# Performance work log

Hardware: AMD Instinct MI355X
Metric: run time of the kernel (lower is better)

The kernel has to match this reference:

```python
import jax, jax.numpy as jnp
import numpy as np
from jax import lax

# sign binarization to {-1,+1} with straight-through estimator (standard BNN binarizePM1)
@jax.custom_vjp
def binarize(x):
    return jnp.where(x >= 0, 1.0, -1.0).astype(x.dtype)

def _bin_fwd(x):
    return binarize(x), None

def _bin_bwd(_, g):
    return (g,)  # straight-through

binarize.defvjp(_bin_fwd, _bin_bwd)

def conv2d(x, w, b):
    # NCHW, OIHW, 3x3, stride 1, pad 1
    y = lax.conv_general_dilated(x, w, window_strides=(1, 1), padding=((1, 1), (1, 1)),
                                 dimension_numbers=('NCHW', 'OIHW', 'NCHW'))
    return y + b[None, :, None, None]

def maxpool2(x):
    return lax.reduce_window(x, -jnp.inf, lax.max, (1, 1, 2, 2), (1, 1, 2, 2), 'VALID')

def bn(x, gamma, beta, mean, var, eps=1e-5):
    # inference-mode batchnorm; broadcasts over channel axis 1 (4D) or feature axis 1 (2D)
    if x.ndim == 4:
        shp = (1, -1, 1, 1)
    else:
        shp = (1, -1)
    inv = gamma * lax.rsqrt(var + eps)
    return x * inv.reshape(shp) + (beta - mean * inv).reshape(shp)

def setup_inputs() -> dict:
    key = jax.random.key(0)
    ks = jax.random.split(key, 16)
    B = 4096
    d = {}
    d['x'] = jax.random.normal(ks[0], (B, 1, 28, 28), jnp.float32)
    d['conv1_w'] = jax.random.normal(ks[1], (64, 1, 3, 3), jnp.float32) * 0.1
    d['conv1_b'] = jax.random.normal(ks[2], (64,), jnp.float32) * 0.01
    d['conv2_w'] = jax.random.normal(ks[3], (64, 64, 3, 3), jnp.float32) * 0.05
    d['conv2_b'] = jax.random.normal(ks[4], (64,), jnp.float32) * 0.01
    d['fc1_w'] = jax.random.normal(ks[5], (2048, 7 * 7 * 64), jnp.float32) * 0.02
    d['fc1_b'] = jax.random.normal(ks[6], (2048,), jnp.float32) * 0.01
    d['fc2_w'] = jax.random.normal(ks[7], (10, 2048), jnp.float32) * 0.02
    d['fc2_b'] = jax.random.normal(ks[8], (10,), jnp.float32) * 0.01
    for i, (name, c) in enumerate([('bn1', 64), ('bn2', 64), ('bn3', 2048)]):
        d[name + '_gamma'] = jnp.ones((c,), jnp.float32)
        d[name + '_beta'] = jnp.zeros((c,), jnp.float32)
        d[name + '_mean'] = jax.random.normal(ks[9 + i], (c,), jnp.float32) * 0.1
        d[name + '_var'] = jax.random.uniform(ks[12 + i], (c,), jnp.float32, 0.5, 1.5)
    d['scale'] = jnp.array([1e-5], jnp.float32)
    return d

def reference(x, conv1_w, conv1_b, conv2_w, conv2_b, fc1_w, fc1_b, fc2_w, fc2_b,
              bn1_gamma, bn1_beta, bn1_mean, bn1_var,
              bn2_gamma, bn2_beta, bn2_mean, bn2_var,
              bn3_gamma, bn3_beta, bn3_mean, bn3_var, scale):
    h = conv2d(x, binarize(conv1_w), conv1_b)          # [B,64,28,28]
    h = maxpool2(h)                                    # [B,64,14,14]
    h = bn(h, bn1_gamma, bn1_beta, bn1_mean, bn1_var)
    h = jnp.clip(h, -1.0, 1.0)                         # hardtanh
    h = binarize(h)                                    # qact1
    h = conv2d(h, binarize(conv2_w), conv2_b)          # [B,64,14,14]
    h = maxpool2(h)                                    # [B,64,7,7]
    h = bn(h, bn2_gamma, bn2_beta, bn2_mean, bn2_var)
    h = jnp.clip(h, -1.0, 1.0)
    h = binarize(h)
    h = h.reshape(h.shape[0], -1)                      # [B,3136]
    h = h @ binarize(fc1_w).T + fc1_b                  # [B,2048]
    h = bn(h, bn3_gamma, bn3_beta, bn3_mean, bn3_var)
    h = jnp.clip(h, -1.0, 1.0)
    h = binarize(h)
    h = h @ binarize(fc2_w).T + fc2_b                  # [B,10]
    return h * scale
```

## Files before the change

kernel.cpp:

```cpp
#include <hip/hip_runtime.h>
#include <stdint.h>

typedef unsigned long long ULL;

__global__ __launch_bounds__(256) void prep_small(const float* __restrict__ w1,
        const float* __restrict__ w2, const float* __restrict__ fc2w,
        float* __restrict__ sgn1, ULL* __restrict__ wb2, ULL* __restrict__ wbf2) {
    int wave = threadIdx.x >> 6, lane = threadIdx.x & 63;
    int W = blockIdx.x * 4 + wave;
    if (W < 576) {
        int co = W / 9, tap = W - co * 9;
        ULL wd = __ballot(w2[(co * 64 + lane) * 9 + tap] >= 0.f);
        if (lane == 0) wb2[W] = wd;
    } else if (W < 896) {
        int idx = W - 576;
        int n = idx >> 5, k = idx & 31;
        ULL wd = __ballot(fc2w[n * 2048 + k * 64 + lane] >= 0.f);
        if (lane == 0) wbf2[idx] = wd;
    } else if (W < 905) {
        int i = (W - 896) * 64 + lane;
        if (i < 576) sgn1[i] = (w1[i] >= 0.f) ? 1.f : -1.f;
    }
}

__global__ __launch_bounds__(256) void prep_pack_fc1(const float* __restrict__ fc1w,
                                                     ULL* __restrict__ wbT) {
    __shared__ float rows[4 * 3136];
    int t = threadIdx.x;
    const float* src = fc1w + (size_t)blockIdx.x * 4 * 3136;
    for (int i = t; i < 4 * 3136; i += 256) rows[i] = src[i];
    __syncthreads();
    int wave = t >> 6, lane = t & 63;
    int n = blockIdx.x * 4 + wave;
    const float* r = rows + wave * 3136 + lane * 49;
    for (int p = 0; p < 49; ++p) {
        ULL wd = __ballot(r[p] >= 0.f);
        if (lane == 0) wbT[p * 2048 + n] = wd;
    }
}

__global__ __launch_bounds__(448, 4) void k1_conv1(const float* __restrict__ x,
        const float* __restrict__ sgn1, const float* __restrict__ b1,
        const float* __restrict__ g, const float* __restrict__ be,
        const float* __restrict__ mu, const float* __restrict__ va,
        ULL* __restrict__ qact1) {
    __shared__ float limg[30 * 30];
    int b = blockIdx.x, t = threadIdx.x;
    int wave = t >> 6, lane = t & 63;
    for (int i = t; i < 900; i += 448) limg[i] = 0.f;
    __syncthreads();
    const float* xb = x + (size_t)b * 784;
    for (int i = t; i < 784; i += 448) {
        int y = i / 28, xx = i - y * 28;
        limg[(xx + 1) * 30 + (y + 1)] = xb[i];
    }
    float w[9];
    #pragma unroll
    for (int k = 0; k < 9; ++k) w[k] = sgn1[lane * 9 + k];
    double iv = (double)g[lane] / sqrt((double)va[lane] + 1e-5);
    double cd = (double)be[lane] - (double)mu[lane] * iv;
    double bd = (double)b1[lane];
    __syncthreads();

    #pragma unroll
    for (int rr = 0; rr < 2; ++rr) {
        int py = wave + rr * 7;
        const float* base = &limg[2 * py];
        #pragma unroll
        for (int px = 0; px < 14; ++px) {
            float a00 = 0.f, a01 = 0.f, a10 = 0.f, a11 = 0.f;
            #pragma unroll
            for (int ky = 0; ky < 3; ++ky) {
                #pragma unroll
                for (int kx = 0; kx < 3; ++kx) {
                    float sv = w[ky * 3 + kx];
                    a00 = fmaf(base[(2 * px + kx)     * 30 + ky],     sv, a00);
                    a01 = fmaf(base[(2 * px + kx + 1) * 30 + ky],     sv, a01);
                    a10 = fmaf(base[(2 * px + kx)     * 30 + ky + 1], sv, a10);
                    a11 = fmaf(base[(2 * px + kx + 1) * 30 + ky + 1], sv, a11);
                }
            }
            float m = fmaxf(fmaxf(a00, a01), fmaxf(a10, a11));
            double v  = (double)m + bd;
            double tt = v * iv + cd;
            ULL word = __ballot(tt >= 0.0);
            if (lane == 0) qact1[(size_t)b * 196 + py * 14 + px] = word;
        }
    }
}

__global__ __launch_bounds__(256, 1) void k2_conv2(const ULL* __restrict__ qact1,
        const ULL* __restrict__ wb2, const float* __restrict__ b2,
        const float* __restrict__ g, const float* __restrict__ be,
        const float* __restrict__ mu, const float* __restrict__ va,
        ULL* __restrict__ qact2) {
    int lane = threadIdx.x & 63;
    int wid = blockIdx.x * 4 + (threadIdx.x >> 6);
    int s = wid / 7, pr = wid - s * 7;

    ULL wk[9];
    #pragma unroll
    for (int k = 0; k < 9; ++k) wk[k] = wb2[lane * 9 + k];
    int pw[9];
    #pragma unroll
    for (int k = 0; k < 9; ++k) pw[k] = 64 - 2 * (int)__popcll(wk[k]);

    double iv   = (double)g[lane] / sqrt((double)va[lane] + 1e-5);
    double cc   = (double)be[lane] - (double)mu[lane] * iv;
    double bias = (double)b2[lane];
    int am, thr;
    if (iv > 0.0) {
        double t0 = -cc / iv - bias;
        int c = (t0 < -590.0) ? -590 : (t0 > 590.0 ? 590 : (int)floor(t0) - 2);
        if (c < -590) c = -590;
        while (c <= 590 && !(((double)c + bias) * iv + cc >= 0.0)) ++c;
        am = 1; thr = c;
    } else if (iv < 0.0) {
        double t0 = -cc / iv - bias;
        int c = (t0 > 590.0) ? 590 : (t0 < -590.0 ? -590 : (int)ceil(t0) + 2);
        if (c > 590) c = 590;
        while (c >= -590 && !(((double)c + bias) * iv + cc >= 0.0)) --c;
        am = -1; thr = c;
    } else {
        am = 1; thr = (cc >= 0.0) ? -1000000 : 1000000;
    }
    int athr = am * thr;

    int corr[2][3];
    #pragma unroll
    for (int j = 0; j < 2; ++j) {
        bool tpad = (pr == 0 && j == 0);
        bool bpad = (pr == 6 && j == 1);
        #pragma unroll
        for (int cls = 0; cls < 3; ++cls) {
            int cacc = 0;
            #pragma unroll
            for (int r = 0; r < 3; ++r) {
                #pragma unroll
                for (int k = 0; k < 3; ++k) {
                    bool pad = (r == 0 && tpad) || (r == 2 && bpad) ||
                               (k == 0 && cls == 0) || (k == 2 && cls == 2);
                    if (pad) cacc += pw[r * 3 + k];
                }
            }
            corr[j][cls] = cacc;
        }
    }

    const ULL* base = qact1 + (size_t)s * 196;
    int r0 = 2 * pr;
    bool top = (pr > 0), bot = (pr < 6);

    ULL cw[4][4];
    #pragma unroll
    for (int r = 0; r < 4; ++r) cw[0][r] = 0ULL;
    #pragma unroll
    for (int c = 0; c < 3; ++c) {
        cw[c + 1][0] = top ? base[(r0 - 1) * 14 + c] : 0ULL;
        cw[c + 1][1] = base[(r0    ) * 14 + c];
        cw[c + 1][2] = base[(r0 + 1) * 14 + c];
        cw[c + 1][3] = bot ? base[(r0 + 2) * 14 + c] : 0ULL;
    }

    #pragma unroll
    for (int px = 0; px < 7; ++px) {
        int s00 = 0, s01 = 0, s10 = 0, s11 = 0;
        #pragma unroll
        for (int ky = 0; ky < 3; ++ky) {
            #pragma unroll
            for (int kx = 0; kx < 3; ++kx) {
                ULL w = wk[ky * 3 + kx];
                s00 += (int)__popcll(cw[kx    ][ky    ] ^ w);
                s01 += (int)__popcll(cw[kx + 1][ky    ] ^ w);
                s10 += (int)__popcll(cw[kx    ][ky + 1] ^ w);
                s11 += (int)__popcll(cw[kx + 1][ky + 1] ^ w);
            }
        }
        const int clsL = (px == 0) ? 0 : 1, clsR = (px == 6) ? 2 : 1;
        int d00 = 576 - 2 * s00 - corr[0][clsL];
        int d01 = 576 - 2 * s01 - corr[0][clsR];
        int d10 = 576 - 2 * s10 - corr[1][clsL];
        int d11 = 576 - 2 * s11 - corr[1][clsR];
        int m = max(max(d00, d01), max(d10, d11));
        ULL word = __ballot(am * m >= athr);
        if (lane == 0) qact2[(size_t)s * 49 + pr * 7 + px] = word;
        if (px < 6) {
            #pragma unroll
            for (int r = 0; r < 4; ++r) { cw[0][r] = cw[2][r]; cw[1][r] = cw[3][r]; }
            #pragma unroll
            for (int c = 0; c < 2; ++c) {
                const int col = 2 * px + 3 + c;
                if (col <= 13) {
                    cw[2 + c][0] = top ? base[(r0 - 1) * 14 + col] : 0ULL;
                    cw[2 + c][1] = base[(r0    ) * 14 + col];
                    cw[2 + c][2] = base[(r0 + 1) * 14 + col];
                    cw[2 + c][3] = bot ? base[(r0 + 2) * 14 + col] : 0ULL;
                } else {
                    cw[2 + c][0] = 0ULL; cw[2 + c][1] = 0ULL;
                    cw[2 + c][2] = 0ULL; cw[2 + c][3] = 0ULL;
                }
            }
        }
    }
}

__global__ __launch_bounds__(256) void k3_fc1(const ULL* __restrict__ qact2,
        const ULL* __restrict__ wbT, const float* __restrict__ fb,
        const float* __restrict__ g, const float* __restrict__ be,
        const float* __restrict__ mu, const float* __restrict__ va,
        ULL* __restrict__ hbits) {
    __shared__ ULL xs[784];
    int t = threadIdx.x, wave = t >> 6, lane = t & 63;
    int b0 = blockIdx.x * 16;
    int gidx = blockIdx.y * 4 + wave;
    int n = gidx * 64 + lane;
    for (int i = t; i < 784; i += 256) xs[i] = qact2[(size_t)b0 * 49 + i];
    double iv   = (double)g[n] / sqrt((double)va[n] + 1e-5);
    double cc   = (double)be[n] - (double)mu[n] * iv;
    double bias = (double)fb[n];
    __syncthreads();
    int acc[16];
    #pragma unroll
    for (int i = 0; i < 16; ++i) acc[i] = 0;
    for (int p = 0; p < 49; ++p) {
        ULL w = wbT[p * 2048 + n];
        #pragma unroll
        for (int i = 0; i < 16; ++i)
            acc[i] += (int)__popcll(xs[i * 49 + p] ^ w);
    }
    #pragma unroll
    for (int i = 0; i < 16; ++i) {
        int dot = 3136 - 2 * acc[i];
        double tt = ((double)dot + bias) * iv + cc;
        ULL word = __ballot(tt >= 0.0);
        if (lane == 0) hbits[(size_t)(b0 + i) * 32 + gidx] = word;
    }
}

__global__ __launch_bounds__(256) void k4_fc2(const ULL* __restrict__ hbits,
        const ULL* __restrict__ wbf2, const float* __restrict__ b2,
        const float* __restrict__ scale, float* __restrict__ out, int total) {
    int gid = blockIdx.x * 256 + threadIdx.x;
    if (gid >= total) return;
    int b = gid / 10, n = gid - b * 10;
    const ULL* h = hbits + (size_t)b * 32;
    const ULL* w = wbf2 + n * 32;
    int acc = 0;
    #pragma unroll
    for (int k = 0; k < 32; ++k) acc += (int)__popcll(h[k] ^ w[k]);
    int dot = 2048 - 2 * acc;
    double v = ((double)dot + (double)b2[n]) * (double)scale[0];
    out[gid] = (float)v;
}

extern "C" void kernel_launch(void* const* d_in, const int* in_sizes, int n_in,
                              void* d_out, int out_size, void* d_ws, size_t ws_size,
                              hipStream_t stream) {
    const float* x      = (const float*)d_in[0];
    const float* w1     = (const float*)d_in[1];
    const float* b1     = (const float*)d_in[2];
    const float* w2     = (const float*)d_in[3];
    const float* b2     = (const float*)d_in[4];
    const float* fc1w   = (const float*)d_in[5];
    const float* fc1b   = (const float*)d_in[6];
    const float* fc2w   = (const float*)d_in[7];
    const float* fc2b   = (const float*)d_in[8];
    const float* g1 = (const float*)d_in[9],  *be1 = (const float*)d_in[10],
               *mu1 = (const float*)d_in[11], *va1 = (const float*)d_in[12];
    const float* g2 = (const float*)d_in[13], *be2 = (const float*)d_in[14],
               *mu2 = (const float*)d_in[15], *va2 = (const float*)d_in[16];
    const float* g3 = (const float*)d_in[17], *be3 = (const float*)d_in[18],
               *mu3 = (const float*)d_in[19], *va3 = (const float*)d_in[20];
    const float* scale = (const float*)d_in[21];
    float* out = (float*)d_out;

    int B = in_sizes[0] / 784;

    char* ws = (char*)d_ws;
    ULL* qact1 = (ULL*)(ws);
    ULL* qact2 = (ULL*)(ws + (size_t)B * 196 * 8);
    ULL* hbits = (ULL*)(ws + (size_t)B * 245 * 8);
    char* wsw  = ws + (size_t)B * 277 * 8;
    ULL* wb2   = (ULL*)(wsw);
    ULL* wbT   = (ULL*)(wsw + 576 * 8);
    ULL* wbf2  = (ULL*)(wsw + 576 * 8 + 49 * 2048 * 8);
    float* sgn1 = (float*)(wsw + 576 * 8 + 49 * 2048 * 8 + 320 * 8);

    prep_small<<<227, 256, 0, stream>>>(w1, w2, fc2w, sgn1, wb2, wbf2);
    prep_pack_fc1<<<512, 256, 0, stream>>>(fc1w, wbT);

    k1_conv1<<<B, 448, 0, stream>>>(x, sgn1, b1, g1, be1, mu1, va1, qact1);
    k2_conv2<<<B * 7 / 4, 256, 0, stream>>>(qact1, wb2, b2, g2, be2, mu2, va2, qact2);
    k3_fc1<<<dim3(B / 16, 8), 256, 0, stream>>>(qact2, wbT, fc1b, g3, be3, mu3, va3, hbits);
    int total = B * 10;
    k4_fc2<<<(total + 255) / 256, 256, 0, stream>>>(hbits, wbf2, fc2b, scale, out, total);
}
```

Before: 306.3 us.

## Process all seven pooled rows per wave in conv2 to amortize weight/threshold setup

```diff
diff --git a/kernel.cpp b/kernel.cpp
--- a/kernel.cpp
+++ b/kernel.cpp
@@ -95,8 +95,7 @@
         const float* __restrict__ mu, const float* __restrict__ va,
         ULL* __restrict__ qact2) {
     int lane = threadIdx.x & 63;
-    int wid = blockIdx.x * 4 + (threadIdx.x >> 6);
-    int s = wid / 7, pr = wid - s * 7;
+    int s = blockIdx.x * 4 + (threadIdx.x >> 6);
 
     ULL wk[9];
     #pragma unroll
@@ -126,78 +125,73 @@
     }
     int athr = am * thr;
 
-    int corr[2][3];
-    #pragma unroll
-    for (int j = 0; j < 2; ++j) {
-        bool tpad = (pr == 0 && j == 0);
-        bool bpad = (pr == 6 && j == 1);
-        #pragma unroll
-        for (int cls = 0; cls < 3; ++cls) {
-            int cacc = 0;
+    int cLs = pw[0] + pw[3] + pw[6], cRs = pw[2] + pw[5] + pw[8];
+    int rT  = pw[0] + pw[1] + pw[2], rB  = pw[6] + pw[7] + pw[8];
+    int tL = cLs + rT - pw[0], tM = rT, tR = cRs + rT - pw[2];
+    int bL = cLs + rB - pw[6], bM = rB, bR = cRs + rB - pw[8];
+
+    const ULL* base = qact1 + (size_t)s * 196;
+    ULL cw[4][4];
+
+    #pragma unroll 1
+    for (int pr = 0; pr < 7; ++pr) {
+        int r0 = 2 * pr;
+        bool tpad = (pr == 0), bpad = (pr == 6);
+        const ULL* rA = base + (tpad ? 0 : (r0 - 1) * 14);
+        const ULL* rB_ = base + r0 * 14;
+        const ULL* rC = base + (r0 + 1) * 14;
+        const ULL* rD = base + (bpad ? 0 : (r0 + 2) * 14);
+        ULL mT = tpad ? 0ULL : ~0ULL;
+        ULL mB = bpad ? 0ULL : ~0ULL;
+        int c00 = tpad ? tL : cLs, c01 = tpad ? tM : 0, c02 = tpad ? tR : cRs;
+        int c10 = bpad ? bL : cLs, c11 = bpad ? bM : 0, c12 = bpad ? bR : cRs;
+
+        #pragma unroll
+        for (int r = 0; r < 4; ++r) cw[0][r] = 0ULL;
+        #pragma unroll
+        for (int c = 0; c < 3; ++c) {
+            cw[c + 1][0] = rA[c] & mT;
+            cw[c + 1][1] = rB_[c];
+            cw[c + 1][2] = rC[c];
+            cw[c + 1][3] = rD[c] & mB;
+        }
+
+        #pragma unroll
+        for (int px = 0; px < 7; ++px) {
+            int s00 = 0, s01 = 0, s10 = 0, s11 = 0;
             #pragma unroll
-            for (int r = 0; r < 3; ++r) {
+            for (int ky = 0; ky < 3; ++ky) {
                 #pragma unroll
-                for (int k = 0; k < 3; ++k) {
-                    bool pad = (r == 0 && tpad) || (r == 2 && bpad) ||
-                               (k == 0 && cls == 0) || (k == 2 && cls == 2);
-                    if (pad) cacc += pw[r * 3 + k];
+                for (int kx = 0; kx < 3; ++kx) {
+                    ULL w = wk[ky * 3 + kx];
+                    s00 += (int)__popcll(cw[(2 * px + kx)     & 3][ky    ] ^ w);
+                    s01 += (int)__popcll(cw[(2 * px + kx + 1) & 3][ky    ] ^ w);
+                    s10 += (int)__popcll(cw[(2 * px + kx)     & 3][ky + 1] ^ w);
+                    s11 += (int)__popcll(cw[(2 * px + kx + 1) & 3][ky + 1] ^ w);
                 }
             }
-            corr[j][cls] = cacc;
-        }
-    }
-
-    const ULL* base = qact1 + (size_t)s * 196;
-    int r0 = 2 * pr;
-    bool top = (pr > 0), bot = (pr < 6);
-
-    ULL cw[4][4];
-    #pragma unroll
-    for (int r = 0; r < 4; ++r) cw[0][r] = 0ULL;
-    #pragma unroll
-    for (int c = 0; c < 3; ++c) {
-        cw[c + 1][0] = top ? base[(r0 - 1) * 14 + c] : 0ULL;
-        cw[c + 1][1] = base[(r0    ) * 14 + c];
-        cw[c + 1][2] = base[(r0 + 1) * 14 + c];
-        cw[c + 1][3] = bot ? base[(r0 + 2) * 14 + c] : 0ULL;
-    }
-
-    #pragma unroll
-    for (int px = 0; px < 7; ++px) {
-        int s00 = 0, s01 = 0, s10 = 0, s11 = 0;
-        #pragma unroll
-        for (int ky = 0; ky < 3; ++ky) {
-            #pragma unroll
-            for (int kx = 0; kx < 3; ++kx) {
-                ULL w = wk[ky * 3 + kx];
-                s00 += (int)__popcll(cw[kx    ][ky    ] ^ w);
-                s01 += (int)__popcll(cw[kx + 1][ky    ] ^ w);
-                s10 += (int)__popcll(cw[kx    ][ky + 1] ^ w);
-                s11 += (int)__popcll(cw[kx + 1][ky + 1] ^ w);
-            }
-        }
-        const int clsL = (px == 0) ? 0 : 1, clsR = (px == 6) ? 2 : 1;
-        int d00 = 576 - 2 * s00 - corr[0][clsL];
-        int d01 = 576 - 2 * s01 - corr[0][clsR];
-        int d10 = 576 - 2 * s10 - corr[1][clsL];
-        int d11 = 576 - 2 * s11 - corr[1][clsR];
-        int m = max(max(d00, d01), max(d10, d11));
-        ULL word = __ballot(am * m >= athr);
-        if (lane == 0) qact2[(size_t)s * 49 + pr * 7 + px] = word;
-        if (px < 6) {
-            #pragma unroll
-            for (int r = 0; r < 4; ++r) { cw[0][r] = cw[2][r]; cw[1][r] = cw[3][r]; }
-            #pragma unroll
-            for (int c = 0; c < 2; ++c) {
-                const int col = 2 * px + 3 + c;
-                if (col <= 13) {
-                    cw[2 + c][0] = top ? base[(r0 - 1) * 14 + col] : 0ULL;
-                    cw[2 + c][1] = base[(r0    ) * 14 + col];
-                    cw[2 + c][2] = base[(r0 + 1) * 14 + col];
-                    cw[2 + c][3] = bot ? base[(r0 + 2) * 14 + col] : 0ULL;
+            int d00 = 576 - 2 * s00 - ((px == 0) ? c00 : c01);
+            int d01 = 576 - 2 * s01 - ((px == 6) ? c02 : c01);
+            int d10 = 576 - 2 * s10 - ((px == 0) ? c10 : c11);
+            int d11 = 576 - 2 * s11 - ((px == 6) ? c12 : c11);
+            int m = max(max(d00, d01), max(d10, d11));
+            ULL word = __ballot(am * m >= athr);
+            if (lane == 0) qact2[(size_t)s * 49 + pr * 7 + px] = word;
+
+            if (px < 6) {
+                const int n1 = 2 * px + 3, n2 = 2 * px + 4;
+                cw[(n1 + 1) & 3][0] = rA[n1] & mT;
+                cw[(n1 + 1) & 3][1] = rB_[n1];
+                cw[(n1 + 1) & 3][2] = rC[n1];
+                cw[(n1 + 1) & 3][3] = rD[n1] & mB;
+                if (n2 <= 13) {
+                    cw[(n2 + 1) & 3][0] = rA[n2] & mT;
+                    cw[(n2 + 1) & 3][1] = rB_[n2];
+                    cw[(n2 + 1) & 3][2] = rC[n2];
+                    cw[(n2 + 1) & 3][3] = rD[n2] & mB;
                 } else {
-                    cw[2 + c][0] = 0ULL; cw[2 + c][1] = 0ULL;
-                    cw[2 + c][2] = 0ULL; cw[2 + c][3] = 0ULL;
+                    #pragma unroll
+                    for (int r = 0; r < 4; ++r) cw[(n2 + 1) & 3][r] = 0ULL;
                 }
             }
         }
@@ -290,7 +284,7 @@
     prep_pack_fc1<<<512, 256, 0, stream>>>(fc1w, wbT);
 
     k1_conv1<<<B, 448, 0, stream>>>(x, sgn1, b1, g1, be1, mu1, va1, qact1);
-    k2_conv2<<<B * 7 / 4, 256, 0, stream>>>(qact1, wb2, b2, g2, be2, mu2, va2, qact2);
+    k2_conv2<<<B / 4, 256, 0, stream>>>(qact1, wb2, b2, g2, be2, mu2, va2, qact2);
     k3_fc1<<<dim3(B / 16, 8), 256, 0, stream>>>(qact2, wbT, fc1b, g3, be3, mu3, va3, hbits);
     int total = B * 10;
     k4_fc2<<<(total + 255) / 256, 256, 0, stream>>>(hbits, wbf2, fc2b, scale, out, total);
```

Measured after the change: 303.2 us. No clear change (-1.0%).
